# Kernel optimization log

Measured on AMD Instinct MI355X. Metric: run time of the kernel, lower is better.

Reference implementation:

```python
import jax, jax.numpy as jnp
import numpy as np

B, S, H = 2, 2048, 1024
E, I, IS, K = 16, 512, 2048, 4


def setup_inputs() -> dict:
    key = jax.random.key(0)
    ks = jax.random.split(key, 8)
    s = 0.02
    return {
        "hidden_states": jax.random.normal(ks[0], (B, S, H), jnp.float32),
        "router_w": jax.random.normal(ks[1], (E, H), jnp.float32) * s,
        "gate_up_proj": jax.random.normal(ks[2], (E, 2 * I, H), jnp.float32) * s,
        "down_proj": jax.random.normal(ks[3], (E, H, I), jnp.float32) * s,
        "shared_gate_w": jax.random.normal(ks[4], (IS, H), jnp.float32) * s,
        "shared_up_w": jax.random.normal(ks[5], (IS, H), jnp.float32) * s,
        "shared_down_w": jax.random.normal(ks[6], (H, IS), jnp.float32) * s,
        "shared_expert_gate_w": jax.random.normal(ks[7], (1, H), jnp.float32) * s,
        "top_k": K,
    }


def reference(hidden_states, router_w, gate_up_proj, down_proj,
              shared_gate_w, shared_up_w, shared_down_w,
              shared_expert_gate_w, top_k):
    b, s, h_dim = hidden_states.shape
    N = b * s
    num_experts = router_w.shape[0]
    h = hidden_states.reshape(N, h_dim)

    # ---- shared expert (SwiGLU MLP) ----
    shared_out = (jax.nn.silu(h @ shared_gate_w.T) * (h @ shared_up_w.T)) @ shared_down_w.T
    shared_out = jax.nn.sigmoid(h @ shared_expert_gate_w.T) * shared_out  # [N, H]

    # ---- router: softmax -> top-k -> renormalize ----
    router_logits = h @ router_w.T  # [N, E]
    router_probs_f32 = jax.nn.softmax(router_logits.astype(jnp.float32), axis=-1)
    top_v, top_i = jax.lax.top_k(router_probs_f32, top_k)  # [N, K]
    top_v = top_v / jnp.sum(top_v, axis=-1, keepdims=True)
    top_v = top_v.astype(router_logits.dtype)

    # combine weights scattered to dense [N, E] (zero for unselected experts)
    one_hot = jax.nn.one_hot(top_i, num_experts, dtype=top_v.dtype)  # [N, K, E]
    combine = jnp.sum(one_hot * top_v[..., None], axis=1)  # [N, E]

    # ---- experts: dense dispatch, masked combine (same math as gather/scatter loop) ----
    gu = jnp.einsum('nh,eih->nei', h, gate_up_proj)  # [N, E, 2I]
    gate, up = jnp.split(gu, 2, axis=-1)
    act = jax.nn.silu(gate) * up  # [N, E, I]
    expert_out = jnp.einsum('nei,ehi,ne->nh', act, down_proj, combine)  # [N, H]

    out = expert_out + shared_out

    # ---- aux load-balancing loss (faithful to source, including its reductions) ----
    tokens_per_expert = jnp.sum(one_hot.astype(jnp.float32), axis=(0, 1))  # [E]
    fraction_tokens = tokens_per_expert / (N * top_k)
    router_probs_sum = jnp.sum(jax.nn.softmax(router_logits, axis=-1), axis=0)  # [E]
    fraction_probs = jnp.sum(router_probs_sum) / N  # scalar (as in source)
    aux_loss = num_experts * jnp.sum(fraction_tokens * fraction_probs)

    return out.reshape(b, s, h_dim), aux_loss
```

## Files before the change

### kernel.cpp

```cpp
#include <hip/hip_runtime.h>

typedef __bf16 bf16_t;
typedef bf16_t bf16x4v __attribute__((ext_vector_type(4)));
typedef bf16_t bf16x8v __attribute__((ext_vector_type(8)));
typedef float f32x4 __attribute__((ext_vector_type(4)));

__device__ __forceinline__ void gl_lds16(const void* g, void* l) {
  __builtin_amdgcn_global_load_lds((__attribute__((address_space(1))) void*)g,
                                   (__attribute__((address_space(3))) void*)l,
                                   16, 0, 0);
}

__device__ __forceinline__ float fast_silu(float x) {
  return x / (1.f + __expf(-x));
}

__global__ void cvt_f32_bf16_kernel(const float* __restrict__ in,
                                    bf16_t* __restrict__ out, int n4) {
  int i = blockIdx.x * blockDim.x + threadIdx.x;
  const int stride = gridDim.x * blockDim.x;
  const float4* in4 = (const float4*)in;
  bf16x4v* out4 = (bf16x4v*)out;
  for (; i < n4; i += stride) {
    float4 v = in4[i];
    bf16x4v o;
    o[0] = (bf16_t)v.x; o[1] = (bf16_t)v.y; o[2] = (bf16_t)v.z; o[3] = (bf16_t)v.w;
    out4[i] = o;
  }
}

__global__ __launch_bounds__(256)
void router_topk_kernel(const float* __restrict__ h, const float* __restrict__ rw,
                        const float* __restrict__ segw, float* __restrict__ gsig,
                        int* __restrict__ tokTopI, float* __restrict__ tokTopW) {
  const int t = threadIdx.x;
  const int lane = t & 63;
  const int wid = t >> 6;
  const int grp = lane >> 4;
  const int e = lane & 15;
  const int tok = blockIdx.x * 16 + wid * 4 + grp;

  const float4* h4 = (const float4*)(h + (size_t)tok * 1024);
  const float4* rw4 = (const float4*)(rw + (size_t)e * 1024);
  const float4* sg4 = (const float4*)segw;

  float s = 0.f, ss = 0.f;
  #pragma unroll 8
  for (int c = 0; c < 256; ++c) {
    float4 hv = h4[c];
    float4 wv = rw4[c];
    s += hv.x * wv.x + hv.y * wv.y + hv.z * wv.z + hv.w * wv.w;
    if ((c & 15) == e) {
      float4 gv = sg4[c];
      ss += hv.x * gv.x + hv.y * gv.y + hv.z * gv.z + hv.w * gv.w;
    }
  }
  #pragma unroll
  for (int m = 1; m <= 8; m <<= 1) ss += __shfl_xor(ss, m);
  float mx = s;
  #pragma unroll
  for (int m = 1; m <= 8; m <<= 1) mx = fmaxf(mx, __shfl_xor(mx, m));
  float p = expf(s - mx);

  float pc = p;
  float tsum = 0.f;
  float myw = 0.f; int myi = 0;
  #pragma unroll
  for (int r = 0; r < 4; ++r) {
    float v = pc; int idx = e;
    #pragma unroll
    for (int m = 1; m <= 8; m <<= 1) {
      float ov = __shfl_xor(v, m); int oi = __shfl_xor(idx, m);
      if (ov > v || (ov == v && oi < idx)) { v = ov; idx = oi; }
    }
    tsum += v;
    if (e == r) { myi = idx; myw = v; }
    if (e == idx) pc = -1.f;
  }
  if (e < 4) {
    tokTopI[tok * 4 + e] = myi;
    tokTopW[tok * 4 + e] = myw / tsum;
  }
  if (e == 0) gsig[tok] = 1.f / (1.f + expf(-ss));
}

__global__ __launch_bounds__(256)
void build_lists_kernel(const int* __restrict__ tokTopI,
                        const float* __restrict__ tokTopW,
                        int* __restrict__ cnt, int* __restrict__ toklist,
                        float* __restrict__ wlist, int* __restrict__ posOf) {
  const int e = blockIdx.x;
  const int t = threadIdx.x;
  const int lane = t & 63;
  const int wid = t >> 6;
  __shared__ int base;
  __shared__ int wsum[4];
  if (t == 0) base = 0;
  __syncthreads();

  for (int chunk = 0; chunk < 16; ++chunk) {
    const int i0 = chunk * 1024 + t * 4;
    int4 ti = *(const int4*)&tokTopI[i0];
    const bool f0 = ti.x == e, f1 = ti.y == e, f2 = ti.z == e, f3 = ti.w == e;
    const int c = (int)f0 + (int)f1 + (int)f2 + (int)f3;
    int inc = c;
    #pragma unroll
    for (int m = 1; m <= 32; m <<= 1) {
      int o = __shfl_up(inc, m);
      if (lane >= m) inc += o;
    }
    const int lanePre = inc - c;
    if (lane == 63) wsum[wid] = inc;
    __syncthreads();
    int wavePre = 0;
    #pragma unroll
    for (int w = 0; w < 4; ++w) if (w < wid) wavePre += wsum[w];
    const int total = wsum[0] + wsum[1] + wsum[2] + wsum[3];
    int pos = base + wavePre + lanePre;
    __syncthreads();
    if (t == 0) base += total;
    float4 tw = *(const float4*)&tokTopW[i0];
    if (f0) { toklist[e * 4096 + pos] = i0 >> 2;       wlist[e * 4096 + pos] = tw.x; posOf[i0]     = pos; pos++; }
    if (f1) { toklist[e * 4096 + pos] = (i0 + 1) >> 2; wlist[e * 4096 + pos] = tw.y; posOf[i0 + 1] = pos; pos++; }
    if (f2) { toklist[e * 4096 + pos] = (i0 + 2) >> 2; wlist[e * 4096 + pos] = tw.z; posOf[i0 + 2] = pos; pos++; }
    if (f3) { toklist[e * 4096 + pos] = (i0 + 3) >> 2; wlist[e * 4096 + pos] = tw.w; posOf[i0 + 3] = pos; pos++; }
  }
  __syncthreads();
  if (t == 0) cnt[e] = base;
}

__global__ void finalize_router_kernel(const int* __restrict__ cnt,
                                       int* __restrict__ baseOff,
                                       float* __restrict__ aux) {
  if (threadIdx.x == 0 && blockIdx.x == 0) {
    int s = 0;
    for (int e = 0; e < 16; ++e) { baseOff[e] = s; s += cnt[e]; }
    aux[0] = 16.0f;
  }
}

template<bool GATHER>
__global__ __launch_bounds__(256, 4)
void gateup_gemm_kernel(const bf16_t* __restrict__ A,
                        const bf16_t* __restrict__ B1,
                        const bf16_t* __restrict__ B2,
                        size_t strideBe,
                        bf16_t* __restrict__ actOut, int ldAct,
                        int K, int Mfixed,
                        const int* __restrict__ cnt,
                        const int* __restrict__ baseOff,
                        const int* __restrict__ toklist) {
  const int e = blockIdx.z;
  const int rowBlk = blockIdx.y, colBlk = blockIdx.x;
  int M, actRowBase;
  if constexpr (GATHER) {
    M = cnt[e];
    if (rowBlk * 128 >= M) return;
    actRowBase = baseOff[e] + rowBlk * 128;
  } else {
    M = Mfixed;
    actRowBase = rowBlk * 128;
  }
  const bf16_t* b1 = B1 + (size_t)e * strideBe;
  const bf16_t* b2 = B2 + (size_t)e * strideBe;

  __shared__ __align__(16) bf16_t As[128 * 64];
  __shared__ __align__(16) bf16_t Bs[128 * 64];

  const int t = threadIdx.x;
  const int sc = (((t & 7) ^ ((t >> 3) & 7))) * 8;

  const bf16_t* aSrc[4];
  const bf16_t* bSrc[4];
  #pragma unroll
  for (int i = 0; i < 4; ++i) {
    int r = (t >> 3) + 32 * i;
    int grow;
    if constexpr (GATHER) {
      int rr = rowBlk * 128 + r;
      grow = (rr < M) ? toklist[e * 4096 + rr] : 0;
    } else {
      grow = rowBlk * 128 + r;
    }
    aSrc[i] = A + (size_t)grow * K + sc;
    int j = colBlk * 64 + (r >> 1);
    bSrc[i] = ((r & 1) ? b2 : b1) + (size_t)j * K + sc;
  }

  f32x4 acc[4][4];
  #pragma unroll
  for (int a = 0; a < 4; ++a)
    #pragma unroll
    for (int b = 0; b < 4; ++b)
      acc[a][b] = (f32x4){0.f, 0.f, 0.f, 0.f};

  const int lane = t & 63;
  const int wid = t >> 6;
  const int wm = wid >> 1, wn = wid & 1;
  const int lr = lane & 15;
  const int lk = (lane >> 4) * 8;

  bf16_t* aDst = As + t * 8;
  bf16_t* bDst = Bs + t * 8;

  for (int k0 = 0; k0 < K; k0 += 64) {
    #pragma unroll
    for (int i = 0; i < 4; ++i) gl_lds16(aSrc[i], aDst + i * 2048);
    #pragma unroll
    for (int i = 0; i < 4; ++i) gl_lds16(bSrc[i], bDst + i * 2048);
    #pragma unroll
    for (int i = 0; i < 4; ++i) { aSrc[i] += 64; bSrc[i] += 64; }
    __syncthreads();
    #pragma unroll
    for (int kk = 0; kk < 64; kk += 32) {
      bf16x8v af[4], bfr[4];
      #pragma unroll
      for (int f = 0; f < 4; ++f) {
        const int row = wm * 64 + f * 16 + lr;
        af[f] = *(const bf16x8v*)&As[row * 64 + ((kk + lk) ^ ((row & 7) << 3))];
      }
      #pragma unroll
      for (int f = 0; f < 4; ++f) {
        const int row = wn * 64 + f * 16 + lr;
        bfr[f] = *(const bf16x8v*)&Bs[row * 64 + ((kk + lk) ^ ((row & 7) << 3))];
      }
      #pragma unroll
      for (int fm = 0; fm < 4; ++fm)
        #pragma unroll
        for (int fn = 0; fn < 4; ++fn)
          acc[fm][fn] = __builtin_amdgcn_mfma_f32_16x16x32_bf16(
              af[fm], bfr[fn], acc[fm][fn], 0, 0, 0);
    }
    __syncthreads();
  }

  const int mRem = M - rowBlk * 128;
  #pragma unroll
  for (int fm = 0; fm < 4; ++fm) {
    #pragma unroll
    for (int fn = 0; fn < 4; ++fn) {
      const int nloc = wn * 64 + fn * 16 + lr;
      const int j = colBlk * 64 + (nloc >> 1);
      const bool even = (nloc & 1) == 0;
      #pragma unroll
      for (int r = 0; r < 4; ++r) {
        float mine = acc[fm][fn][r];
        float other = __shfl_xor(mine, 1);
        float gate = even ? mine : other;
        float up = even ? other : mine;
        float act = fast_silu(gate) * up;
        int tr = wm * 64 + fm * 16 + (lane >> 4) * 4 + r;
        if (even && tr < mRem)
          actOut[(size_t)(actRowBase + tr) * ldAct + j] = (bf16_t)act;
      }
    }
  }
}

template<bool EXPERT>
__global__ __launch_bounds__(256, 4)
void down_gemm_kernel(const bf16_t* __restrict__ Abase,
                      const bf16_t* __restrict__ Bbase,
                      size_t strideBe,
                      float* __restrict__ outF,
                      bf16_t* __restrict__ outB,
                      const float* __restrict__ gsig,
                      int K, int Mfixed,
                      const int* __restrict__ cnt,
                      const int* __restrict__ baseOff,
                      const float* __restrict__ wlist) {
  const int e = blockIdx.z;
  const int rowBlk = blockIdx.y, colBlk = blockIdx.x;
  int M, aRowBase;
  const bf16_t* A;
  if constexpr (EXPERT) {
    M = cnt[e];
    if (rowBlk * 128 >= M) return;
    aRowBase = baseOff[e] + rowBlk * 128;
    A = Abase + (size_t)baseOff[e] * K;
  } else {
    M = Mfixed;
    aRowBase = rowBlk * 128;
    A = Abase;
  }
  const bf16_t* B = Bbase + (size_t)e * strideBe;

  __shared__ __align__(16) bf16_t As[128 * 64];
  __shared__ __align__(16) bf16_t Bs[128 * 64];

  const int t = threadIdx.x;
  const int sc = (((t & 7) ^ ((t >> 3) & 7))) * 8;
  const bf16_t* aSrc[4];
  const bf16_t* bSrc[4];
  #pragma unroll
  for (int i = 0; i < 4; ++i) {
    int r = (t >> 3) + 32 * i;
    aSrc[i] = A + (size_t)(rowBlk * 128 + r) * K + sc;
    bSrc[i] = B + (size_t)(colBlk * 128 + r) * K + sc;
  }

  f32x4 acc[4][4];
  #pragma unroll
  for (int a = 0; a < 4; ++a)
    #pragma unroll
    for (int b = 0; b < 4; ++b)
      acc[a][b] = (f32x4){0.f, 0.f, 0.f, 0.f};

  const int lane = t & 63;
  const int wid = t >> 6;
  const int wm = wid >> 1, wn = wid & 1;
  const int lr = lane & 15;
  const int lk = (lane >> 4) * 8;

  bf16_t* aDst = As + t * 8;
  bf16_t* bDst = Bs + t * 8;

  for (int k0 = 0; k0 < K; k0 += 64) {
    #pragma unroll
    for (int i = 0; i < 4; ++i) gl_lds16(aSrc[i], aDst + i * 2048);
    #pragma unroll
    for (int i = 0; i < 4; ++i) gl_lds16(bSrc[i], bDst + i * 2048);
    #pragma unroll
    for (int i = 0; i < 4; ++i) { aSrc[i] += 64; bSrc[i] += 64; }
    __syncthreads();
    #pragma unroll
    for (int kk = 0; kk < 64; kk += 32) {
      bf16x8v af[4], bfr[4];
      #pragma unroll
      for (int f = 0; f < 4; ++f) {
        const int row = wm * 64 + f * 16 + lr;
        af[f] = *(const bf16x8v*)&As[row * 64 + ((kk + lk) ^ ((row & 7) << 3))];
      }
      #pragma unroll
      for (int f = 0; f < 4; ++f) {
        const int row = wn * 64 + f * 16 + lr;
        bfr[f] = *(const bf16x8v*)&Bs[row * 64 + ((kk + lk) ^ ((row & 7) << 3))];
      }
      #pragma unroll
      for (int fm = 0; fm < 4; ++fm)
        #pragma unroll
        for (int fn = 0; fn < 4; ++fn)
          acc[fm][fn] = __builtin_amdgcn_mfma_f32_16x16x32_bf16(
              af[fm], bfr[fn], acc[fm][fn], 0, 0, 0);
    }
    __syncthreads();
  }

  const int mRem = M - rowBlk * 128;
  #pragma unroll
  for (int fm = 0; fm < 4; ++fm) {
    #pragma unroll
    for (int r = 0; r < 4; ++r) {
      const int tr = wm * 64 + fm * 16 + (lane >> 4) * 4 + r;
      if (tr < mRem) {
        float wgt;
        if constexpr (EXPERT) wgt = wlist[e * 4096 + rowBlk * 128 + tr];
        else                  wgt = gsig[rowBlk * 128 + tr];
        #pragma unroll
        for (int fn = 0; fn < 4; ++fn) {
          const int col = colBlk * 128 + wn * 64 + fn * 16 + lr;
          float v = acc[fm][fn][r] * wgt;
          if constexpr (EXPERT)
            outB[(size_t)(aRowBase + tr) * 1024 + col] = (bf16_t)v;
          else
            outF[(size_t)(aRowBase + tr) * 1024 + col] = v;
        }
      }
    }
  }
}

__global__ __launch_bounds__(256)
void combine_kernel(const bf16_t* __restrict__ dsc,
                    const int* __restrict__ tokTopI,
                    const int* __restrict__ posOf,
                    const int* __restrict__ baseOff,
                    float* __restrict__ out) {
  const int tok = blockIdx.x;
  const int t = threadIdx.x;
  __shared__ const bf16_t* rows[4];
  if (t < 4) {
    int e = tokTopI[tok * 4 + t];
    rows[t] = dsc + (size_t)(baseOff[e] + posOf[tok * 4 + t]) * 1024;
  }
  __syncthreads();
  float4* orow = (float4*)(out + (size_t)tok * 1024);
  float4 v = orow[t];
  #pragma unroll
  for (int k = 0; k < 4; ++k) {
    bf16x4v b = *(const bf16x4v*)(rows[k] + t * 4);
    v.x += (float)b[0]; v.y += (float)b[1]; v.z += (float)b[2]; v.w += (float)b[3];
  }
  orow[t] = v;
}


extern "C" void kernel_launch(void* const* d_in, const int* in_sizes, int n_in,
                              void* d_out, int out_size, void* d_ws, size_t ws_size,
                              hipStream_t stream) {
  const float* h_f32 = (const float*)d_in[0];
  const float* rw    = (const float*)d_in[1];
  const float* gup   = (const float*)d_in[2];
  const float* dwn   = (const float*)d_in[3];
  const float* sgate = (const float*)d_in[4];
  const float* sup   = (const float*)d_in[5];
  const float* sdown = (const float*)d_in[6];
  const float* segw  = (const float*)d_in[7];

  char* ws = (char*)d_ws;
  bf16_t* h_bf    = (bf16_t*)(ws + 0);
  bf16_t* gup_bf  = (bf16_t*)(ws + 8388608);
  bf16_t* dwn_bf  = (bf16_t*)(ws + 41943040);
  bf16_t* sg_bf   = (bf16_t*)(ws + 58720256);
  bf16_t* su_bf   = (bf16_t*)(ws + 62914560);
  bf16_t* sd_bf   = (bf16_t*)(ws + 67108864);
  bf16_t* act_s   = (bf16_t*)(ws + 71303168);
  bf16_t* act_e   = (bf16_t*)(ws + 88080384);
  float*  gsig    = (float*)(ws + 105119744);
  int*    cnt     = (int*)(ws + 105136128);
  int*    baseOff = (int*)(ws + 105136384);
  int*    toklist = (int*)(ws + 105136640);
  float*  wlist   = (float*)(ws + 105398784);
  int*    tokTopI = (int*)(ws + 105660928);
  float*  tokTopW = (float*)(ws + 105726464);
  int*    posOf   = (int*)(ws + 105791744);
  bf16_t* dsc     = gup_bf;

  float* out = (float*)d_out;
  float* aux = out + 4194304;

  auto cvtLaunch = [&](const float* src, bf16_t* dst, int n) {
    int n4 = n / 4;
    int blocks = (n4 + 255) / 256;
    if (blocks > 2048) blocks = 2048;
    cvt_f32_bf16_kernel<<<blocks, 256, 0, stream>>>(src, dst, n4);
  };
  cvtLaunch(h_f32, h_bf, 4194304);
  cvtLaunch(gup,   gup_bf, 16777216);
  cvtLaunch(dwn,   dwn_bf, 8388608);
  cvtLaunch(sgate, sg_bf, 2097152);
  cvtLaunch(sup,   su_bf, 2097152);
  cvtLaunch(sdown, sd_bf, 2097152);

  router_topk_kernel<<<256, 256, 0, stream>>>(h_f32, rw, segw, gsig, tokTopI, tokTopW);
  build_lists_kernel<<<16, 256, 0, stream>>>(tokTopI, tokTopW, cnt, toklist, wlist, posOf);
  finalize_router_kernel<<<1, 64, 0, stream>>>(cnt, baseOff, aux);

  gateup_gemm_kernel<false><<<dim3(32, 32, 1), 256, 0, stream>>>(
      h_bf, sg_bf, su_bf, (size_t)0, act_s, 2048, 1024, 4096,
      nullptr, nullptr, nullptr);
  gateup_gemm_kernel<true><<<dim3(8, 32, 16), 256, 0, stream>>>(
      h_bf, gup_bf, gup_bf + 512 * 1024, (size_t)1024 * 1024, act_e, 512, 1024, 0,
      cnt, baseOff, toklist);
  down_gemm_kernel<false><<<dim3(8, 32, 1), 256, 0, stream>>>(
      act_s, sd_bf, (size_t)0, out, nullptr, gsig, 2048, 4096,
      nullptr, nullptr, nullptr);
  down_gemm_kernel<true><<<dim3(8, 32, 16), 256, 0, stream>>>(
      act_e, dwn_bf, (size_t)1024 * 512, nullptr, dsc, nullptr, 512, 0,
      cnt, baseOff, wlist);
  combine_kernel<<<4096, 256, 0, stream>>>(dsc, tokTopI, posOf, baseOff, out);
}
```

Measured before the change: 459.9 us.

## Merge conversion launches and fuse shared/routed expert GEMMs into single grids

Replaces six separate f32-to-bf16 conversion launches with one kernel that walks all tensors in a single index space. It also merges the shared-expert and routed-expert gate/up GEMMs into one launch (z<16 routed, z>=16 shared), and does the same for the down GEMMs. The aim is to cut launch overhead and tail idle time between dependent small kernels, letting shared and routed work fill the GPU together. In exchange, template specialisation becomes runtime branching, with dynamic K and extra branch logic in the hot kernels, which may cost registers or occupancy.

```diff
diff --git a/kernel.cpp b/kernel.cpp
--- a/kernel.cpp
+++ b/kernel.cpp
@@ -15,17 +15,27 @@
   return x / (1.f + __expf(-x));
 }
 
-__global__ void cvt_f32_bf16_kernel(const float* __restrict__ in,
-                                    bf16_t* __restrict__ out, int n4) {
-  int i = blockIdx.x * blockDim.x + threadIdx.x;
-  const int stride = gridDim.x * blockDim.x;
-  const float4* in4 = (const float4*)in;
-  bf16x4v* out4 = (bf16x4v*)out;
-  for (; i < n4; i += stride) {
-    float4 v = in4[i];
+__global__ __launch_bounds__(256)
+void cvt_all_kernel(const float* __restrict__ h, const float* __restrict__ gup,
+                    const float* __restrict__ dwn, const float* __restrict__ sg,
+                    const float* __restrict__ su, const float* __restrict__ sd,
+                    bf16_t* __restrict__ h_bf, bf16_t* __restrict__ gup_bf,
+                    bf16_t* __restrict__ dwn_bf, bf16_t* __restrict__ sg_bf,
+                    bf16_t* __restrict__ su_bf, bf16_t* __restrict__ sd_bf) {
+  int i = blockIdx.x * 256 + threadIdx.x;
+  const int stride = gridDim.x * 256;
+  for (; i < 8912896; i += stride) {
+    const float4* src; bf16x4v* dst; int off;
+    if (i < 1048576)      { src = (const float4*)h;   dst = (bf16x4v*)h_bf;   off = i; }
+    else if (i < 5242880) { src = (const float4*)gup; dst = (bf16x4v*)gup_bf; off = i - 1048576; }
+    else if (i < 7340032) { src = (const float4*)dwn; dst = (bf16x4v*)dwn_bf; off = i - 5242880; }
+    else if (i < 7864320) { src = (const float4*)sg;  dst = (bf16x4v*)sg_bf;  off = i - 7340032; }
+    else if (i < 8388608) { src = (const float4*)su;  dst = (bf16x4v*)su_bf;  off = i - 7864320; }
+    else                  { src = (const float4*)sd;  dst = (bf16x4v*)sd_bf;  off = i - 8388608; }
+    float4 v = src[off];
     bf16x4v o;
     o[0] = (bf16_t)v.x; o[1] = (bf16_t)v.y; o[2] = (bf16_t)v.z; o[3] = (bf16_t)v.w;
-    out4[i] = o;
+    dst[off] = o;
   }
 }
 
@@ -139,52 +149,58 @@
   }
 }
 
-template<bool GATHER>
 __global__ __launch_bounds__(256, 4)
-void gateup_gemm_kernel(const bf16_t* __restrict__ A,
-                        const bf16_t* __restrict__ B1,
-                        const bf16_t* __restrict__ B2,
-                        size_t strideBe,
-                        bf16_t* __restrict__ actOut, int ldAct,
-                        int K, int Mfixed,
-                        const int* __restrict__ cnt,
-                        const int* __restrict__ baseOff,
-                        const int* __restrict__ toklist) {
-  const int e = blockIdx.z;
-  const int rowBlk = blockIdx.y, colBlk = blockIdx.x;
-  int M, actRowBase;
-  if constexpr (GATHER) {
-    M = cnt[e];
+void gateup_merged_kernel(const bf16_t* __restrict__ h_bf,
+                          const bf16_t* __restrict__ gup_bf,
+                          const bf16_t* __restrict__ sg_bf,
+                          const bf16_t* __restrict__ su_bf,
+                          bf16_t* __restrict__ act_e,
+                          bf16_t* __restrict__ act_s,
+                          const int* __restrict__ cnt,
+                          const int* __restrict__ baseOff,
+                          const int* __restrict__ toklist) {
+  const int z = blockIdx.z;
+  const int rowBlk = blockIdx.y;
+  const bool routed = (z < 16);
+
+  int M, actRowBase, colBlk, ldAct;
+  const bf16_t *b1, *b2;
+  const int* gather;
+  bf16_t* actOut;
+  if (routed) {
+    M = cnt[z];
     if (rowBlk * 128 >= M) return;
-    actRowBase = baseOff[e] + rowBlk * 128;
+    actRowBase = baseOff[z] + rowBlk * 128;
+    colBlk = blockIdx.x;
+    b1 = gup_bf + (size_t)z * 1048576;
+    b2 = b1 + 524288;
+    gather = toklist + z * 4096;
+    actOut = act_e; ldAct = 512;
   } else {
-    M = Mfixed;
+    M = 4096;
     actRowBase = rowBlk * 128;
-  }
-  const bf16_t* b1 = B1 + (size_t)e * strideBe;
-  const bf16_t* b2 = B2 + (size_t)e * strideBe;
+    colBlk = (z - 16) * 8 + blockIdx.x;
+    b1 = sg_bf; b2 = su_bf;
+    gather = nullptr;
+    actOut = act_s; ldAct = 2048;
+  }
 
   __shared__ __align__(16) bf16_t As[128 * 64];
   __shared__ __align__(16) bf16_t Bs[128 * 64];
 
   const int t = threadIdx.x;
-  const int sc = (((t & 7) ^ ((t >> 3) & 7))) * 8;
+  const int sc = ((t & 7) ^ ((t >> 3) & 7)) * 8;
 
   const bf16_t* aSrc[4];
   const bf16_t* bSrc[4];
   #pragma unroll
   for (int i = 0; i < 4; ++i) {
     int r = (t >> 3) + 32 * i;
-    int grow;
-    if constexpr (GATHER) {
-      int rr = rowBlk * 128 + r;
-      grow = (rr < M) ? toklist[e * 4096 + rr] : 0;
-    } else {
-      grow = rowBlk * 128 + r;
-    }
-    aSrc[i] = A + (size_t)grow * K + sc;
+    int rr = rowBlk * 128 + r;
+    int grow = routed ? ((rr < M) ? gather[rr] : 0) : rr;
+    aSrc[i] = h_bf + (size_t)grow * 1024 + sc;
     int j = colBlk * 64 + (r >> 1);
-    bSrc[i] = ((r & 1) ? b2 : b1) + (size_t)j * K + sc;
+    bSrc[i] = ((r & 1) ? b2 : b1) + (size_t)j * 1024 + sc;
   }
 
   f32x4 acc[4][4];
@@ -203,7 +219,7 @@
   bf16_t* aDst = As + t * 8;
   bf16_t* bDst = Bs + t * 8;
 
-  for (int k0 = 0; k0 < K; k0 += 64) {
+  for (int k0 = 0; k0 < 1024; k0 += 64) {
     #pragma unroll
     for (int i = 0; i < 4; ++i) gl_lds16(aSrc[i], aDst + i * 2048);
     #pragma unroll
@@ -257,39 +273,42 @@
   }
 }
 
-template<bool EXPERT>
 __global__ __launch_bounds__(256, 4)
-void down_gemm_kernel(const bf16_t* __restrict__ Abase,
-                      const bf16_t* __restrict__ Bbase,
-                      size_t strideBe,
-                      float* __restrict__ outF,
-                      bf16_t* __restrict__ outB,
-                      const float* __restrict__ gsig,
-                      int K, int Mfixed,
-                      const int* __restrict__ cnt,
-                      const int* __restrict__ baseOff,
-                      const float* __restrict__ wlist) {
-  const int e = blockIdx.z;
+void down_merged_kernel(const bf16_t* __restrict__ act_e,
+                        const bf16_t* __restrict__ act_s,
+                        const bf16_t* __restrict__ dwn_bf,
+                        const bf16_t* __restrict__ sd_bf,
+                        float* __restrict__ outF,
+                        bf16_t* __restrict__ dsc,
+                        const float* __restrict__ gsig,
+                        const int* __restrict__ cnt,
+                        const int* __restrict__ baseOff,
+                        const float* __restrict__ wlist) {
+  const int z = blockIdx.z;
   const int rowBlk = blockIdx.y, colBlk = blockIdx.x;
-  int M, aRowBase;
-  const bf16_t* A;
-  if constexpr (EXPERT) {
-    M = cnt[e];
+  const bool routed = (z < 16);
+
+  int M, K, aRowBase;
+  const bf16_t *A, *B;
+  if (routed) {
+    M = cnt[z];
     if (rowBlk * 128 >= M) return;
-    aRowBase = baseOff[e] + rowBlk * 128;
-    A = Abase + (size_t)baseOff[e] * K;
+    K = 512;
+    aRowBase = baseOff[z] + rowBlk * 128;
+    A = act_e + (size_t)baseOff[z] * 512;
+    B = dwn_bf + (size_t)z * 524288;
   } else {
-    M = Mfixed;
+    M = 4096; K = 2048;
     aRowBase = rowBlk * 128;
-    A = Abase;
-  }
-  const bf16_t* B = Bbase + (size_t)e * strideBe;
+    A = act_s;
+    B = sd_bf;
+  }
 
   __shared__ __align__(16) bf16_t As[128 * 64];
   __shared__ __align__(16) bf16_t Bs[128 * 64];
 
   const int t = threadIdx.x;
-  const int sc = (((t & 7) ^ ((t >> 3) & 7))) * 8;
+  const int sc = ((t & 7) ^ ((t >> 3) & 7)) * 8;
   const bf16_t* aSrc[4];
   const bf16_t* bSrc[4];
   #pragma unroll
@@ -354,14 +373,14 @@
       const int tr = wm * 64 + fm * 16 + (lane >> 4) * 4 + r;
       if (tr < mRem) {
         float wgt;
-        if constexpr (EXPERT) wgt = wlist[e * 4096 + rowBlk * 128 + tr];
-        else                  wgt = gsig[rowBlk * 128 + tr];
+        if (routed) wgt = wlist[z * 4096 + rowBlk * 128 + tr];
+        else        wgt = gsig[rowBlk * 128 + tr];
         #pragma unroll
         for (int fn = 0; fn < 4; ++fn) {
           const int col = colBlk * 128 + wn * 64 + fn * 16 + lr;
           float v = acc[fm][fn][r] * wgt;
-          if constexpr (EXPERT)
-            outB[(size_t)(aRowBase + tr) * 1024 + col] = (bf16_t)v;
+          if (routed)
+            dsc[(size_t)(aRowBase + tr) * 1024 + col] = (bf16_t)v;
           else
             outF[(size_t)(aRowBase + tr) * 1024 + col] = v;
         }
@@ -429,34 +448,18 @@
   float* out = (float*)d_out;
   float* aux = out + 4194304;
 
-  auto cvtLaunch = [&](const float* src, bf16_t* dst, int n) {
-    int n4 = n / 4;
-    int blocks = (n4 + 255) / 256;
-    if (blocks > 2048) blocks = 2048;
-    cvt_f32_bf16_kernel<<<blocks, 256, 0, stream>>>(src, dst, n4);
-  };
-  cvtLaunch(h_f32, h_bf, 4194304);
-  cvtLaunch(gup,   gup_bf, 16777216);
-  cvtLaunch(dwn,   dwn_bf, 8388608);
-  cvtLaunch(sgate, sg_bf, 2097152);
-  cvtLaunch(sup,   su_bf, 2097152);
-  cvtLaunch(sdown, sd_bf, 2097152);
+  cvt_all_kernel<<<4096, 256, 0, stream>>>(h_f32, gup, dwn, sgate, sup, sdown,
+                                           h_bf, gup_bf, dwn_bf, sg_bf, su_bf, sd_bf);
 
   router_topk_kernel<<<256, 256, 0, stream>>>(h_f32, rw, segw, gsig, tokTopI, tokTopW);
   build_lists_kernel<<<16, 256, 0, stream>>>(tokTopI, tokTopW, cnt, toklist, wlist, posOf);
   finalize_router_kernel<<<1, 64, 0, stream>>>(cnt, baseOff, aux);
 
-  gateup_gemm_kernel<false><<<dim3(32, 32, 1), 256, 0, stream>>>(
-      h_bf, sg_bf, su_bf, (size_t)0, act_s, 2048, 1024, 4096,
-      nullptr, nullptr, nullptr);
-  gateup_gemm_kernel<true><<<dim3(8, 32, 16), 256, 0, stream>>>(
-      h_bf, gup_bf, gup_bf + 512 * 1024, (size_t)1024 * 1024, act_e, 512, 1024, 0,
-      cnt, baseOff, toklist);
-  down_gemm_kernel<false><<<dim3(8, 32, 1), 256, 0, stream>>>(
-      act_s, sd_bf, (size_t)0, out, nullptr, gsig, 2048, 4096,
-      nullptr, nullptr, nullptr);
-  down_gemm_kernel<true><<<dim3(8, 32, 16), 256, 0, stream>>>(
-      act_e, dwn_bf, (size_t)1024 * 512, nullptr, dsc, nullptr, 512, 0,
-      cnt, baseOff, wlist);
+  gateup_merged_kernel<<<dim3(8, 32, 20), 256, 0, stream>>>(
+      h_bf, gup_bf, sg_bf, su_bf, act_e, act_s, cnt, baseOff, toklist);
+
+  down_merged_kernel<<<dim3(8, 32, 17), 256, 0, stream>>>(
+      act_e, act_s, dwn_bf, sd_bf, out, dsc, gsig, cnt, baseOff, wlist);
+
   combine_kernel<<<4096, 256, 0, stream>>>(dsc, tokTopI, posOf, baseOff, out);
 }
```

Measured after the change: 492.3 us. 7.0% more time.
